# Kernel optimization log

Measured on AMD Instinct MI355X. Metric: run time of the kernel, lower is better.

The kernel has to match this reference:

```python
import jax, jax.numpy as jnp
import numpy as np

B, T, M_DIM, P_DIM = 32, 192, 256, 16
D, HE, HD, HG = 1024, 1024, 1024, 512
NH, DH, DFF, NL = 16, 64, 4096, 8
CTX = 10
E = P_DIM // 2  # num_experts = d_phase // 2
PRELU_A = 0.25  # torch PReLU default init slope (treated as constant)
LN_EPS = 1e-5


def prelu(x):
    return jnp.where(x >= 0, x, PRELU_A * x)


def layer_norm(x, g, b):
    m = x.mean(-1, keepdims=True)
    v = ((x - m) ** 2).mean(-1, keepdims=True)
    return (x - m) * jax.lax.rsqrt(v + LN_EPS) * g + b


def setup_inputs() -> dict:
    key = jax.random.key(0)
    ks = iter(jax.random.split(key, 64))
    w = lambda *s: jax.random.normal(next(ks), s, jnp.float32) * 0.02
    return dict(
        motion=jax.random.normal(next(ks), (B, T, M_DIM), jnp.float32),
        phase=jax.random.normal(next(ks), (B, T, P_DIM), jnp.float32),
        enc_W1=w(M_DIM + 1 + P_DIM, HE), enc_b1=w(HE), enc_W2=w(HE, D), enc_b2=w(D),
        kf_W1=w(2, D), kf_b1=w(D), kf_W2=w(D, D), kf_b2=w(D),
        rp_W1=w(1, DH), rp_b1=w(DH), rp_W2=w(DH, DH), rp_b2=w(DH),
        att_Wq=w(NL, D, NH * DH), att_bq=w(NL, NH * DH),
        att_Wk=w(NL, D, NH * DH), att_bk=w(NL, NH * DH),
        att_Wv=w(NL, D, NH * DH), att_bv=w(NL, NH * DH),
        att_Wo=w(NL, NH * DH, D), att_bo=w(NL, D),
        att_ln_g=jnp.ones((NL, D)), att_ln_b=jnp.zeros((NL, D)),
        pff_W1=w(NL, D, DFF), pff_b1=w(NL, DFF),
        pff_W2=w(NL, DFF, D), pff_b2=w(NL, D),
        pff_ln_g=jnp.ones((NL, D)), pff_ln_b=jnp.zeros((NL, D)),
        fin_ln_g=jnp.ones(D), fin_ln_b=jnp.zeros(D),
        pd_W1=w(D, HD), pd_b1=w(HD), pd_W2=w(HD, P_DIM), pd_b2=w(P_DIM),
        g_W1=w(P_DIM, HG), g_b1=w(HG), g_W2=w(HG, HG), g_b2=w(HG),
        g_W3=w(HG, E), g_b3=w(E),
        md_W0=w(E, D, HD), md_b0=w(E, HD),
        md_W1=w(E, HD, HD), md_b1=w(E, HD),
        md_W2=w(E, HD, M_DIM), md_b2=w(E, M_DIM),
    )


def reference(motion, phase, enc_W1, enc_b1, enc_W2, enc_b2,
              kf_W1, kf_b1, kf_W2, kf_b2, rp_W1, rp_b1, rp_W2, rp_b2,
              att_Wq, att_bq, att_Wk, att_bk, att_Wv, att_bv, att_Wo, att_bo,
              att_ln_g, att_ln_b, pff_W1, pff_b1, pff_W2, pff_b2, pff_ln_g, pff_ln_b,
              fin_ln_g, fin_ln_b, pd_W1, pd_b1, pd_W2, pd_b2,
              g_W1, g_b1, g_W2, g_b2, g_W3, g_b3,
              md_W0, md_b0, md_W1, md_b1, md_W2, md_b2):
    frames = jnp.arange(T)
    # eval mode: no midway targets; keyframes = context frames + last frame
    key_mask = (frames < CTX) | (frames == T - 1)          # [T]
    dm = key_mask.astype(motion.dtype)[:, None]            # data mask [T,1]
    x = jnp.concatenate([motion * dm,
                         jnp.broadcast_to(dm, (B, T, 1)),
                         phase * dm], axis=-1)
    x = prelu(x @ enc_W1 + enc_b1)
    x = prelu(x @ enc_W2 + enc_b2)                          # [B,T,D]
    # keyframe position embedding (distance to last context / target frame)
    ctx_idx = (frames - (CTX - 1)).astype(x.dtype)
    tgt_idx = -(frames - (T - 1)).astype(x.dtype)
    kp = jnp.stack([ctx_idx, tgt_idx], axis=-1)            # [T,2]
    x = x + (prelu(kp @ kf_W1 + kf_b1) @ kf_W2 + kf_b2)
    # relative position embedding, offsets -(T-1)..(T-1)
    rp = jnp.arange(-T + 1, T, dtype=x.dtype)[:, None]     # [2T-1,1]
    rel = prelu(rp @ rp_W1 + rp_b1) @ rp_W2 + rp_b2        # [2T-1,DH]
    rel_idx = frames[None, :] - frames[:, None] + (T - 1)  # [T,T] -> index into 2T-1
    blocked = ~key_mask                                    # attention mask: only attend to keyframes
    neg = jnp.asarray(-1e9, x.dtype)
    scale = 1.0 / np.sqrt(DH)

    def block(x, p):
        Wq, bq, Wk, bk, Wv, bv, Wo, bo, lg, lb, pW1, pb1, pW2, pb2, plg, plb = p
        h = layer_norm(x, lg, lb)                          # pre_lnorm
        q = (h @ Wq + bq).reshape(B, T, NH, DH)
        k = (h @ Wk + bk).reshape(B, T, NH, DH)
        v = (h @ Wv + bv).reshape(B, T, NH, DH)
        ac = jnp.einsum('bind,bjnd->bnij', q, k)           # content score
        bd = jnp.einsum('bind,rd->bnir', q, rel)           # rel-pos score (shared across heads' rel emb)
        bd = jnp.take_along_axis(bd, jnp.broadcast_to(rel_idx[None, None], ac.shape), axis=-1)
        s = (ac + bd) * scale
        s = jnp.where(blocked[None, None, None, :], neg, s)
        a = jax.nn.softmax(s, axis=-1)
        o = jnp.einsum('bnij,bjnd->bind', a, v).reshape(B, T, NH * DH)
        x = x + o @ Wo + bo
        h2 = layer_norm(x, plg, plb)
        x = x + jax.nn.relu(h2 @ pW1 + pb1) @ pW2 + pb2    # positionwise FF
        return x, None

    layer_params = (att_Wq, att_bq, att_Wk, att_bk, att_Wv, att_bv, att_Wo, att_bo,
                    att_ln_g, att_ln_b, pff_W1, pff_b1, pff_W2, pff_b2, pff_ln_g, pff_ln_b)
    x, _ = jax.lax.scan(block, x, layer_params)
    x = layer_norm(x, fin_ln_g, fin_ln_b)                  # final LN (pre_lnorm)
    # phase decoder
    phase_out = prelu(x @ pd_W1 + pd_b1) @ pd_W2 + pd_b2   # [B,T,P]
    # gating network -> per-frame soft expert weights
    h = prelu(phase_out @ g_W1 + g_b1)
    h = prelu(h @ g_W2 + g_b2)
    gate = jax.nn.softmax(h @ g_W3 + g_b3, axis=-1)        # [B,T,E]

    def mlin(y, W, b):
        # MultiLinear + per-frame expert blend: sum_e gate_e * (y @ W_e + b_e)
        return jnp.einsum('btd,edh,bte->bth', y, W, gate) + jnp.einsum('bte,eh->bth', gate, b)

    y = prelu(mlin(x, md_W0, md_b0))
    y = prelu(mlin(y, md_W1, md_b1))
    y = mlin(y, md_W2, md_b2)                              # [B,T,M]
    return y, phase_out
```

## Files before the change

### kernel.cpp

```cpp
#include <hip/hip_runtime.h>
#include <stdint.h>

typedef unsigned short u16;
typedef __attribute__((ext_vector_type(4))) float f32x4;
typedef __attribute__((ext_vector_type(8))) __bf16 bf16x8;

#define NT 6144
#define TT 192
#define PRELU_A 0.25f

__device__ __forceinline__ u16 f2bf(float f) {
  unsigned u = __float_as_uint(f);
  u += 0x7fffu + ((u >> 16) & 1u);
  return (u16)(u >> 16);
}
__device__ __forceinline__ float bf2f(u16 u) {
  return __uint_as_float(((unsigned)u) << 16);
}

__device__ __forceinline__ void gload16(const u16* g, __bf16* l) {
  auto* l3 = reinterpret_cast<__attribute__((address_space(3))) __bf16*>(
      reinterpret_cast<uintptr_t>(l));
  const auto* g1 = reinterpret_cast<const __attribute__((address_space(1))) u16*>(
      reinterpret_cast<uintptr_t>(g));
  __builtin_amdgcn_global_load_lds(g1, l3, 16, 0, 0);
}

__device__ __forceinline__ void xcd_remap(int& bx, int& by)
{
  const int gx = gridDim.x, gy = gridDim.y;
  const int nwg = gx * gy;
  const int f = blockIdx.y * gx + blockIdx.x;
  const int q = nwg >> 3, r = nwg & 7;
  const int xcd = f & 7, s = f >> 3;
  const int w = (xcd < r ? xcd*(q+1) : r*(q+1) + (xcd-r)*q) + s;
  const int CX = ((gx & 7) == 0) ? (gx >> 3) : 1;
  const int per = gy * CX;
  const int c = w / per, rr = w - c*per;
  bx = c*CX + (rr % CX);
  by = rr / CX;
}

struct TrDesc {
  const float* src; u16* dst;
  int K, N, Kp, Np;
  int tilesX, perBatch, batch, tileOff;
  long sstride, dstride;
};
struct TrTable { TrDesc d[18]; int n; };

__global__ __launch_bounds__(256)
void transpose_all(TrTable T)
{
  __shared__ float tile[64][65];
  const int bid = blockIdx.x;
  TrDesc de;
  #pragma unroll 1
  for (int i = 0; i < T.n; ++i) {
    const TrDesc& e = T.d[i];
    if (bid >= e.tileOff && bid < e.tileOff + e.perBatch * e.batch) { de = e; break; }
  }
  const int local = bid - de.tileOff;
  const int z = local / de.perBatch;
  const int rem = local - z * de.perBatch;
  const int ty = rem / de.tilesX;
  const int tx = rem - ty * de.tilesX;
  const float* src = de.src + (long)z * de.sstride;
  u16* dst = de.dst + (long)z * de.dstride;
  const int kt = ty * 64, nt2 = tx * 64;

  if (kt + 64 <= de.K && nt2 + 64 <= de.N) {
    #pragma unroll
    for (int i = 0; i < 4; ++i) {
      const int flat = threadIdx.x + i*256;
      const int ng = (flat & 7) | (((flat >> 9) & 1) << 3);
      const int kl = ((flat >> 3) & 7) | (((flat >> 6) & 7) << 3);
      const float4 v = *(const float4*)(src + (long)(kt + kl)*de.N + nt2 + ng*4);
      *(float4*)&tile[kl][ng*4] = v;
    }
  } else {
    #pragma unroll
    for (int i = 0; i < 16; ++i) {
      int idx = threadIdx.x + i*256;
      int kl = idx >> 6, nl = idx & 63;
      int k = kt + kl, n = nt2 + nl;
      tile[kl][nl] = (k < de.K && n < de.N) ? src[(long)k*de.N + n] : 0.f;
    }
  }
  __syncthreads();
  #pragma unroll
  for (int i = 0; i < 4; ++i) {
    const int flat = threadIdx.x + i*256;
    const int kg = (flat & 7) | (((flat >> 5) & 1) << 3);
    const int nl = ((flat >> 3) & 3) | (((flat >> 6) & 15) << 2);
    ushort4 o;
    o.x = f2bf(tile[kg*4 + 0][nl]);
    o.y = f2bf(tile[kg*4 + 1][nl]);
    o.z = f2bf(tile[kg*4 + 2][nl]);
    o.w = f2bf(tile[kg*4 + 3][nl]);
    *(ushort4*)(dst + (long)(nt2 + nl)*de.Kp + kt + kg*4) = o;
  }
}

template<int MR, int HM>
__device__ __forceinline__ void epilogue_store(
    f32x4 (&acc)[MR][4], long arow0, long brow0, int wm, int wn, int lane,
    const float* bias, int biasN,
    float* Cf, int ldc, int Nf, int accum,
    u16* Cb, int ldcb, int Nb, int act, const float* radd)
{
  const int rbase = wm*HM + ((lane >> 4) << 2);
  const int cbase = wn*64 + (lane & 15);
  #pragma unroll
  for (int m = 0; m < MR; ++m) {
    #pragma unroll
    for (int n = 0; n < 4; ++n) {
      const long gcol = brow0 + cbase + n*16;
      const float bv = (bias && gcol < biasN) ? bias[gcol] : 0.f;
      #pragma unroll
      for (int r = 0; r < 4; ++r) {
        const long grow = arow0 + rbase + m*16 + r;
        float v = acc[m][n][r] + bv;
        if (act == 1) v = fmaxf(v, 0.f);
        else if (act == 2) v = (v >= 0.f) ? v : PRELU_A * v;
        if (radd) v += radd[(int)(grow % TT)*1024 + gcol];
        if (Cf && gcol < Nf) {
          const long idx = grow * (long)ldc + gcol;
          Cf[idx] = accum ? (Cf[idx] + v) : v;
        }
        if (Cb && gcol < Nb) Cb[grow * (long)ldcb + gcol] = f2bf(v);
      }
    }
  }
}

__global__ __launch_bounds__(256, 3)
void gemm64(const u16* __restrict__ A, const u16* __restrict__ Bt,
            const float* __restrict__ bias, int biasN,
            float* __restrict__ Cf, int ldc, int Nf, int accum,
            u16* __restrict__ Cb, int ldcb, int Nb,
            int K, int act, const float* __restrict__ radd)
{
  __shared__ __bf16 As[2*64*64];
  __shared__ __bf16 Bs[2*128*64];
  const int tid = threadIdx.x;
  const int wid = tid >> 6;
  const int lane = tid & 63;
  const int wm = wid >> 1, wn = wid & 1;
  int bx, by; xcd_remap(bx, by);
  const long arow0 = (long)bx * 64;
  const long brow0 = (long)by * 128;
  const int lr  = lane >> 3;
  const int lko = ((lane & 7) ^ (lane >> 3)) << 3;

  f32x4 acc[2][4];
  #pragma unroll
  for (int m = 0; m < 2; ++m)
    #pragma unroll
    for (int n = 0; n < 4; ++n) acc[m][n] = (f32x4)0.f;

  const int aro = lane & 15;
  const int g = lane >> 4;

  auto stage = [&](int buf, int kt) {
    #pragma unroll
    for (int c = wid; c < 24; c += 4) {
      if (c < 8) gload16(A + (arow0 + c*8 + lr)*K + kt + lko, As + buf*(64*64) + c*512);
      else       gload16(Bt + (brow0 + (c-8)*8 + lr)*K + kt + lko,
                         Bs + buf*(128*64) + (c-8)*512);
    }
  };

  const int nt = K >> 6;
  stage(0, 0);
  for (int t = 0; t < nt; ++t) {
    if (t + 1 < nt) {
      stage((t+1) & 1, (t+1) << 6);
      asm volatile("s_waitcnt vmcnt(6)" ::: "memory");
    } else {
      asm volatile("s_waitcnt vmcnt(0)" ::: "memory");
    }
    __builtin_amdgcn_s_barrier();
    asm volatile("" ::: "memory");
    const __bf16* Ab = As + (t&1)*(64*64);
    const __bf16* Bb = Bs + (t&1)*(128*64);
    #pragma unroll
    for (int kk = 0; kk < 2; ++kk) {
      bf16x8 af[2], bfv[4];
      #pragma unroll
      for (int m = 0; m < 2; ++m) {
        const int R = wm*32 + m*16 + aro;
        af[m] = *(const bf16x8*)(Ab + R*64 + (((kk*4 + g) ^ (R & 7)) << 3));
      }
      #pragma unroll
      for (int n = 0; n < 4; ++n) {
        const int R = wn*64 + n*16 + aro;
        bfv[n] = *(const bf16x8*)(Bb + R*64 + (((kk*4 + g) ^ (R & 7)) << 3));
      }
      #pragma unroll
      for (int m = 0; m < 2; ++m)
        #pragma unroll
        for (int n = 0; n < 4; ++n)
          acc[m][n] = __builtin_amdgcn_mfma_f32_16x16x32_bf16(af[m], bfv[n], acc[m][n], 0, 0, 0);
    }
    asm volatile("" ::: "memory");
    __builtin_amdgcn_s_barrier();
  }
  epilogue_store<2,32>(acc, arow0, brow0, wm, wn, lane,
                       bias, biasN, Cf, ldc, Nf, accum, Cb, ldcb, Nb, act, radd);
}

__global__ __launch_bounds__(256, 4)
void gemm128(const u16* __restrict__ A, const u16* __restrict__ Bt,
             const float* __restrict__ bias, int biasN,
             float* __restrict__ Cf, int ldc, int Nf, int accum,
             u16* __restrict__ Cb, int ldcb, int Nb,
             int K, int act)
{
  __shared__ __bf16 As[2*128*32];
  __shared__ __bf16 Bs[2*128*32];
  const int tid = threadIdx.x;
  const int wid = tid >> 6;
  const int lane = tid & 63;
  const int wm = wid >> 1, wn = wid & 1;
  int bx, by; xcd_remap(bx, by);
  const long arow0 = (long)bx * 128;
  const long brow0 = (long)by * 128;
  const int srow = lane >> 2;
  const int skoff = ((lane & 3) ^ ((lane >> 3) & 3)) << 3;

  f32x4 acc[4][4];
  #pragma unroll
  for (int m = 0; m < 4; ++m)
    #pragma unroll
    for (int n = 0; n < 4; ++n) acc[m][n] = (f32x4)0.f;

  const int aro = lane & 15;
  const int g = lane >> 4;

  auto stage = [&](int buf, int kt) {
    #pragma unroll
    for (int c = wid; c < 16; c += 4) {
      if (c < 8) gload16(A + (arow0 + c*16 + srow)*K + kt + skoff, As + buf*4096 + c*512);
      else       gload16(Bt + (brow0 + (c-8)*16 + srow)*K + kt + skoff,
                         Bs + buf*4096 + (c-8)*512);
    }
  };

  const int nt = K >> 5;
  stage(0, 0);
  for (int t = 0; t < nt; ++t) {
    if (t + 1 < nt) {
      stage((t+1) & 1, (t+1) << 5);
      asm volatile("s_waitcnt vmcnt(4)" ::: "memory");
    } else {
      asm volatile("s_waitcnt vmcnt(0)" ::: "memory");
    }
    __builtin_amdgcn_s_barrier();
    asm volatile("" ::: "memory");
    const __bf16* Ab = As + (t&1)*4096;
    const __bf16* Bb = Bs + (t&1)*4096;
    bf16x8 af[4], bfv[4];
    #pragma unroll
    for (int m = 0; m < 4; ++m) {
      const int R = wm*64 + m*16 + aro;
      af[m] = *(const bf16x8*)(Ab + R*32 + ((g ^ ((R >> 1) & 3)) << 3));
    }
    #pragma unroll
    for (int n = 0; n < 4; ++n) {
      const int R = wn*64 + n*16 + aro;
      bfv[n] = *(const bf16x8*)(Bb + R*32 + ((g ^ ((R >> 1) & 3)) << 3));
    }
    #pragma unroll
    for (int m = 0; m < 4; ++m)
      #pragma unroll
      for (int n = 0; n < 4; ++n)
        acc[m][n] = __builtin_amdgcn_mfma_f32_16x16x32_bf16(af[m], bfv[n], acc[m][n], 0, 0, 0);
    asm volatile("" ::: "memory");
    __builtin_amdgcn_s_barrier();
  }
  epilogue_store<4,64>(acc, arow0, brow0, wm, wn, lane,
                       bias, biasN, Cf, ldc, Nf, accum, Cb, ldcb, Nb, act, nullptr);
}

__global__ __launch_bounds__(256)
void moe_blend2(const u16* __restrict__ C0, const u16* __restrict__ C1,
                const float* __restrict__ gate, u16* __restrict__ outb)
{
  const long idx = (long)blockIdx.x*256 + threadIdx.x;
  if (idx >= (long)NT*256) return;
  const long t = idx >> 8;
  const int h = (int)(idx & 255) << 2;
  float sx = 0.f, sy = 0.f, sz = 0.f, sw = 0.f;
  #pragma unroll
  for (int j = 0; j < 4; ++j) {
    const float gv = gate[t*8 + j];
    const ushort4 c4 = *(const ushort4*)(C0 + t*4096 + j*1024 + h);
    sx += gv * bf2f(c4.x); sy += gv * bf2f(c4.y);
    sz += gv * bf2f(c4.z); sw += gv * bf2f(c4.w);
  }
  #pragma unroll
  for (int j = 0; j < 4; ++j) {
    const float gv = gate[t*8 + 4 + j];
    const ushort4 c4 = *(const ushort4*)(C1 + t*4096 + j*1024 + h);
    sx += gv * bf2f(c4.x); sy += gv * bf2f(c4.y);
    sz += gv * bf2f(c4.z); sw += gv * bf2f(c4.w);
  }
  sx = (sx >= 0.f) ? sx : PRELU_A * sx;
  sy = (sy >= 0.f) ? sy : PRELU_A * sy;
  sz = (sz >= 0.f) ? sz : PRELU_A * sz;
  sw = (sw >= 0.f) ? sw : PRELU_A * sw;
  ushort4 o; o.x = f2bf(sx); o.y = f2bf(sy); o.z = f2bf(sz); o.w = f2bf(sw);
  *(ushort4*)(outb + t*1024 + h) = o;
}

__global__ __launch_bounds__(256)
void moe_blend_out(const u16* __restrict__ C, const float* __restrict__ gate,
                   float* __restrict__ outf)
{
  const long idx = (long)blockIdx.x*256 + threadIdx.x;
  if (idx >= (long)NT*64) return;
  const long t = idx >> 6;
  const int h = (int)(idx & 63) << 2;
  float sx = 0.f, sy = 0.f, sz = 0.f, sw = 0.f;
  #pragma unroll
  for (int j = 0; j < 8; ++j) {
    const float gv = gate[t*8 + j];
    const ushort4 c4 = *(const ushort4*)(C + t*2048 + j*256 + h);
    sx += gv * bf2f(c4.x); sy += gv * bf2f(c4.y);
    sz += gv * bf2f(c4.z); sw += gv * bf2f(c4.w);
  }
  float4 o; o.x = sx; o.y = sy; o.z = sz; o.w = sw;
  ((float4*)(outf + t*256))[h >> 2] = o;
}

__global__ __launch_bounds__(256)
void build_xin(const float* __restrict__ motion, const float* __restrict__ phase,
               u16* __restrict__ xin)
{
  const long idx = (long)blockIdx.x*256 + threadIdx.x;
  if (idx >= (long)NT*320) return;
  const int c = (int)(idx % 320);
  const long row = idx / 320;
  const int t = (int)(row % TT);
  const bool dm = (t < 10) || (t == TT-1);
  float v;
  if (c < 256)       v = dm ? motion[row*256 + c] : 0.f;
  else if (c == 256) v = dm ? 1.f : 0.f;
  else if (c < 273)  v = dm ? phase[row*16 + (c-257)] : 0.f;
  else               v = 0.f;
  xin[idx] = f2bf(v);
}

__global__ __launch_bounds__(256)
void build_kp_kvb(u16* __restrict__ kp,
                  const float* __restrict__ bk, const float* __restrict__ bv,
                  float* __restrict__ kvb)
{
  const int idx = blockIdx.x*256 + threadIdx.x;
  if (idx < 256*64) {
    const int r = idx / 64, c = idx % 64;
    float v = 0.f;
    if (r < TT) {
      if (c == 0) v = (float)(r - 9);
      else if (c == 1) v = (float)(TT-1 - r);
    }
    kp[idx] = f2bf(v);
  } else {
    const int j = idx - 256*64;
    if (j < 8*2048) {
      const int l = j >> 11, c = j & 2047;
      kvb[j] = (c < 1024) ? bk[l*1024 + c] : bv[l*1024 + c - 1024];
    }
  }
}

__global__ __launch_bounds__(64)
void relpos(const float* __restrict__ W1, const float* __restrict__ b1,
            const float* __restrict__ W2, const float* __restrict__ b2,
            float* __restrict__ rel)
{
  const int r = blockIdx.x;
  const int d = threadIdx.x;
  __shared__ float h[64];
  const float rp = (float)(r - (TT-1));
  float hv = rp * W1[d] + b1[d];
  hv = (hv >= 0.f) ? hv : PRELU_A * hv;
  h[d] = hv;
  __syncthreads();
  if (r < 2*TT - 1) {
    float o = b2[d];
    for (int j = 0; j < 64; ++j) o += h[j] * W2[j*64 + d];
    rel[r*64 + d] = o;
  } else {
    rel[r*64 + d] = 0.f;
  }
}

__global__ __launch_bounds__(256)
void ln_bf16(const float* __restrict__ x, const float* __restrict__ g,
             const float* __restrict__ b, u16* __restrict__ out,
             u16* __restrict__ hk)
{
  const long row = blockIdx.x;
  const float4 v = ((const float4*)(x + row*1024))[threadIdx.x];
  float s  = v.x + v.y + v.z + v.w;
  float s2 = v.x*v.x + v.y*v.y + v.z*v.z + v.w*v.w;
  #pragma unroll
  for (int m = 32; m; m >>= 1) { s += __shfl_xor(s, m); s2 += __shfl_xor(s2, m); }
  __shared__ float red[8];
  const int wid = threadIdx.x >> 6;
  if ((threadIdx.x & 63) == 0) { red[wid] = s; red[wid+4] = s2; }
  __syncthreads();
  s  = red[0] + red[1] + red[2] + red[3];
  s2 = red[4] + red[5] + red[6] + red[7];
  const float mean = s * (1.f/1024.f);
  const float var  = fmaxf(s2 * (1.f/1024.f) - mean*mean, 0.f);
  const float rs   = rsqrtf(var + 1e-5f);
  const float4 gg = ((const float4*)g)[threadIdx.x];
  const float4 bb = ((const float4*)b)[threadIdx.x];
  ushort4 o;
  o.x = f2bf((v.x-mean)*rs*gg.x + bb.x);
  o.y = f2bf((v.y-mean)*rs*gg.y + bb.y);
  o.z = f2bf((v.z-mean)*rs*gg.z + bb.z);
  o.w = f2bf((v.w-mean)*rs*gg.w + bb.w);
  ((ushort4*)(out + row*1024))[threadIdx.x] = o;
  if (hk) {
    const int t = (int)(row % TT);
    if (t < 10 || t == TT-1) {
      const int bidx = (int)(row / TT);
      const int j = (t < 10) ? t : 10;
      ((ushort4*)(hk + (long)(bidx*11 + j)*1024))[threadIdx.x] = o;
    }
  }
}

__global__ __launch_bounds__(256)
void attn11(const float* __restrict__ q, const float* __restrict__ kv,
            const float* __restrict__ rel, u16* __restrict__ o)
{
  const int row = blockIdx.x;
  const int b = row / TT, i = row - b*TT;
  const int t = threadIdx.x;
  const int n = t >> 4;
  const int dq = t & 15;
  const float4 qv = *(const float4*)(q + (long)row*1024 + t*4);
  float e[11];
  float mx = -1e30f;
  #pragma unroll
  for (int j = 0; j < 11; ++j) {
    const int kf = (j < 10) ? j : (TT-1);
    const float4 k4 = *(const float4*)(kv + (long)(b*11 + j)*2048 + n*64 + dq*4);
    const float4 r4 = *(const float4*)(rel + (kf - i + TT-1)*64 + dq*4);
    float s = qv.x*(k4.x+r4.x) + qv.y*(k4.y+r4.y)
            + qv.z*(k4.z+r4.z) + qv.w*(k4.w+r4.w);
    s += __shfl_xor(s, 1); s += __shfl_xor(s, 2);
    s += __shfl_xor(s, 4); s += __shfl_xor(s, 8);
    e[j] = s * 0.125f;
    mx = fmaxf(mx, e[j]);
  }
  float den = 0.f;
  #pragma unroll
  for (int j = 0; j < 11; ++j) { e[j] = __expf(e[j] - mx); den += e[j]; }
  const float inv = 1.f / den;
  float ax = 0.f, ay = 0.f, az = 0.f, aw = 0.f;
  #pragma unroll
  for (int j = 0; j < 11; ++j) {
    const float4 v4 = *(const float4*)(kv + (long)(b*11 + j)*2048 + 1024 + n*64 + dq*4);
    ax += e[j]*v4.x; ay += e[j]*v4.y; az += e[j]*v4.z; aw += e[j]*v4.w;
  }
  ushort4 ov;
  ov.x = f2bf(ax*inv); ov.y = f2bf(ay*inv); ov.z = f2bf(az*inv); ov.w = f2bf(aw*inv);
  *(ushort4*)(o + (long)row*1024 + t*4) = ov;
}

__global__ __launch_bounds__(256)
void softmax8(const float* __restrict__ lg, float* __restrict__ gate)
{
  const int t = blockIdx.x*256 + threadIdx.x;
  if (t >= NT) return;
  float v[8], mx = -1e30f;
  #pragma unroll
  for (int e = 0; e < 8; ++e) { v[e] = lg[t*8 + e]; mx = fmaxf(mx, v[e]); }
  float den = 0.f;
  #pragma unroll
  for (int e = 0; e < 8; ++e) { v[e] = __expf(v[e] - mx); den += v[e]; }
  const float inv = 1.f / den;
  #pragma unroll
  for (int e = 0; e < 8; ++e) gate[t*8 + e] = v[e] * inv;
}

extern "C" void kernel_launch(void* const* d_in, const int* in_sizes, int n_in,
                              void* d_out, int out_size, void* d_ws, size_t ws_size,
                              hipStream_t stream)
{
  (void)in_sizes; (void)n_in; (void)out_size; (void)ws_size;
  const float* motion  = (const float*)d_in[0];
  const float* phase   = (const float*)d_in[1];
  const float* enc_W1  = (const float*)d_in[2];
  const float* enc_b1  = (const float*)d_in[3];
  const float* enc_W2  = (const float*)d_in[4];
  const float* enc_b2  = (const float*)d_in[5];
  const float* kf_W1   = (const float*)d_in[6];
  const float* kf_b1   = (const float*)d_in[7];
  const float* kf_W2   = (const float*)d_in[8];
  const float* kf_b2   = (const float*)d_in[9];
  const float* rp_W1   = (const float*)d_in[10];
  const float* rp_b1   = (const float*)d_in[11];
  const float* rp_W2   = (const float*)d_in[12];
  const float* rp_b2   = (const float*)d_in[13];
  const float* att_Wq  = (const float*)d_in[14];
  const float* att_bq  = (const float*)d_in[15];
  const float* att_Wk  = (const float*)d_in[16];
  const float* att_bk  = (const float*)d_in[17];
  const float* att_Wv  = (const float*)d_in[18];
  const float* att_bv  = (const float*)d_in[19];
  const float* att_Wo  = (const float*)d_in[20];
  const float* att_bo  = (const float*)d_in[21];
  const float* att_ln_g = (const float*)d_in[22];
  const float* att_ln_b = (const float*)d_in[23];
  const float* pff_W1  = (const float*)d_in[24];
  const float* pff_b1  = (const float*)d_in[25];
  const float* pff_W2  = (const float*)d_in[26];
  const float* pff_b2  = (const float*)d_in[27];
  const float* pff_ln_g = (const float*)d_in[28];
  const float* pff_ln_b = (const float*)d_in[29];
  const float* fin_ln_g = (const float*)d_in[30];
  const float* fin_ln_b = (const float*)d_in[31];
  const float* pd_W1   = (const float*)d_in[32];
  const float* pd_b1   = (const float*)d_in[33];
  const float* pd_W2   = (const float*)d_in[34];
  const float* pd_b2   = (const float*)d_in[35];
  const float* g_W1    = (const float*)d_in[36];
  const float* g_b1    = (const float*)d_in[37];
  const float* g_W2    = (const float*)d_in[38];
  const float* g_b2    = (const float*)d_in[39];
  const float* g_W3    = (const float*)d_in[40];
  const float* g_b3    = (const float*)d_in[41];
  const float* md_W0   = (const float*)d_in[42];
  const float* md_b0   = (const float*)d_in[43];
  const float* md_W1   = (const float*)d_in[44];
  const float* md_b1   = (const float*)d_in[45];
  const float* md_W2   = (const float*)d_in[46];
  const float* md_b2   = (const float*)d_in[47];

  char* wsp = (char*)d_ws;
  size_t off = 0;
  auto alloc = [&](size_t bytes) -> char* {
    char* p = wsp + off;
    off += (bytes + 255) & ~(size_t)255;
    return p;
  };

  u16* encW1T = (u16*)alloc((size_t)1024*320*2);
  u16* encW2T = (u16*)alloc((size_t)1024*1024*2);
  u16* kfW1T  = (u16*)alloc((size_t)1024*64*2);
  u16* kfW2T  = (u16*)alloc((size_t)1024*1024*2);
  u16* WqT    = (u16*)alloc((size_t)8*1024*1024*2);
  u16* kvT    = (u16*)alloc((size_t)8*2048*1024*2);
  u16* WoT    = (u16*)alloc((size_t)8*1024*1024*2);
  u16* F1T    = (u16*)alloc((size_t)8*4096*1024*2);
  u16* F2T    = (u16*)alloc((size_t)8*1024*4096*2);
  u16* pdW1T  = (u16*)alloc((size_t)1024*1024*2);
  u16* pdW2T  = (u16*)alloc((size_t)128*1024*2);
  u16* gW1T   = (u16*)alloc((size_t)512*64*2);
  u16* gW2T   = (u16*)alloc((size_t)512*512*2);
  u16* gW3T   = (u16*)alloc((size_t)128*512*2);
  u16* md0T   = (u16*)alloc((size_t)8*1024*1024*2);
  u16* md1T   = (u16*)alloc((size_t)8*1024*1024*2);
  u16* md2T   = (u16*)alloc((size_t)8*256*1024*2);

  float* x    = (float*)alloc((size_t)NT*1024*4);
  float* rel  = (float*)alloc((size_t)384*64*4);
  u16*   kp   = (u16*)  alloc((size_t)256*64*2);
  u16*   kf1  = (u16*)  alloc((size_t)256*1024*2);
  float* kfe  = (float*)alloc((size_t)256*1024*4);
  u16*   hk   = (u16*)  alloc((size_t)384*1024*2);
  float* kvb  = (float*)alloc((size_t)8*2048*4);
  float* kvbuf= (float*)alloc((size_t)384*2048*4);
  u16*   phbf = (u16*)  alloc((size_t)NT*64*2);
  float* glog = (float*)alloc((size_t)NT*8*4);
  float* gate = (float*)alloc((size_t)NT*8*4);
  u16*   xin  = (u16*)  alloc((size_t)NT*320*2);
  u16*   s1   = (u16*)  alloc((size_t)NT*1024*2);
  float* s2   = (float*)alloc((size_t)NT*1024*4);
  u16*   s3   = (u16*)  alloc((size_t)NT*1024*2);
  u16*   s4   = (u16*)  alloc((size_t)NT*4096*2);
  u16*   s5   = (u16*)  alloc((size_t)NT*4096*2);

  float* outY = (float*)d_out;
  float* outP = outY + (size_t)NT*256;

  auto g64 = [&](const u16* A, const u16* Bt, const float* bias, int biasN,
                 float* Cf, int ldc, int Nf, int accum,
                 u16* Cb, int ldcb, int Nb, int M, int K, int Npad, int act,
                 const float* radd) {
    gemm64<<<dim3(M/64, Npad/128), 256, 0, stream>>>(
        A, Bt, bias, biasN, Cf, ldc, Nf, accum, Cb, ldcb, Nb, K, act, radd);
  };
  auto g128 = [&](const u16* A, const u16* Bt, const float* bias, int biasN,
                  float* Cf, int ldc, int Nf, int accum,
                  u16* Cb, int ldcb, int Nb, int M, int K, int Npad, int act) {
    gemm128<<<dim3(M/128, Npad/128), 256, 0, stream>>>(
        A, Bt, bias, biasN, Cf, ldc, Nf, accum, Cb, ldcb, Nb, K, act);
  };

  TrTable T;
  int tn = 0, toff = 0;
  auto addtr = [&](const float* s_, u16* d_, int K, int N, int Kp, int Np,
                   int batch, long dstride) {
    TrDesc& e = T.d[tn++];
    e.src = s_; e.dst = d_; e.K = K; e.N = N; e.Kp = Kp; e.Np = Np;
    e.tilesX = (Np + 63) / 64;
    e.perBatch = e.tilesX * ((Kp + 63) / 64);
    e.batch = batch; e.tileOff = toff;
    e.sstride = (long)K * N; e.dstride = dstride;
    toff += e.perBatch * batch;
  };
  addtr(enc_W1, encW1T, 273, 1024, 320, 1024, 1, (long)1024*320);
  addtr(enc_W2, encW2T, 1024, 1024, 1024, 1024, 1, (long)1024*1024);
  addtr(kf_W1,  kfW1T,  2, 1024, 64, 1024, 1, (long)1024*64);
  addtr(kf_W2,  kfW2T,  1024, 1024, 1024, 1024, 1, (long)1024*1024);
  addtr(att_Wq, WqT, 1024, 1024, 1024, 1024, 8, (long)1024*1024);
  addtr(att_Wk, kvT,                      1024, 1024, 1024, 1024, 8, (long)2048*1024);
  addtr(att_Wv, kvT + (size_t)1024*1024,  1024, 1024, 1024, 1024, 8, (long)2048*1024);
  addtr(att_Wo, WoT, 1024, 1024, 1024, 1024, 8, (long)1024*1024);
  addtr(pff_W1, F1T, 1024, 4096, 1024, 4096, 8, (long)4096*1024);
  addtr(pff_W2, F2T, 4096, 1024, 4096, 1024, 8, (long)1024*4096);
  addtr(pd_W1,  pdW1T, 1024, 1024, 1024, 1024, 1, (long)1024*1024);
  addtr(pd_W2,  pdW2T, 1024, 16, 1024, 128, 1, (long)128*1024);
  addtr(g_W1,   gW1T, 16, 512, 64, 512, 1, (long)512*64);
  addtr(g_W2,   gW2T, 512, 512, 512, 512, 1, (long)512*512);
  addtr(g_W3,   gW3T, 512, 8, 512, 128, 1, (long)128*512);
  addtr(md_W0,  md0T, 1024, 1024, 1024, 1024, 8, (long)1024*1024);
  addtr(md_W1,  md1T, 1024, 1024, 1024, 1024, 8, (long)1024*1024);
  addtr(md_W2,  md2T, 1024, 256, 1024, 256, 8, (long)256*1024);
  T.n = tn;
  transpose_all<<<toff, 256, 0, stream>>>(T);

  build_xin<<<(NT*320 + 255)/256, 256, 0, stream>>>(motion, phase, xin);
  build_kp_kvb<<<(256*64 + 8*2048 + 255)/256, 256, 0, stream>>>(kp, att_bk, att_bv, kvb);
  relpos<<<384, 64, 0, stream>>>(rp_W1, rp_b1, rp_W2, rp_b2, rel);

  g64(kp,  kfW1T, kf_b1, 1024, nullptr,0,0,0, kf1,1024,1024, 256, 64, 1024, 2, nullptr);
  g64(kf1, kfW2T, kf_b2, 1024, kfe,1024,1024,0, nullptr,0,0, 256, 1024, 1024, 0, nullptr);
  g64(xin, encW1T, enc_b1, 1024, nullptr,0,0,0, s1,1024,1024, NT, 320, 1024, 2, nullptr);
  g64(s1,  encW2T, enc_b2, 1024, x,1024,1024,0, nullptr,0,0, NT, 1024, 1024, 2, kfe);

  for (int l = 0; l < 8; ++l) {
    const size_t w1 = (size_t)l*1024*1024;
    const size_t wf = (size_t)l*4096*1024;
    ln_bf16<<<NT, 256, 0, stream>>>(x, att_ln_g + l*1024, att_ln_b + l*1024, s1, hk);
    g64(s1, WqT + w1, att_bq + l*1024, 1024, s2,1024,1024,0, nullptr,0,0, NT, 1024, 1024, 0, nullptr);
    g64(hk, kvT + (size_t)l*2048*1024, kvb + l*2048, 2048,
        kvbuf,2048,2048,0, nullptr,0,0, 384, 1024, 2048, 0, nullptr);
    attn11<<<NT, 256, 0, stream>>>(s2, kvbuf, rel, s3);
    g64(s3, WoT + w1, att_bo + l*1024, 1024, x,1024,1024,1, nullptr,0,0, NT, 1024, 1024, 0, nullptr);
    ln_bf16<<<NT, 256, 0, stream>>>(x, pff_ln_g + l*1024, pff_ln_b + l*1024, s1, nullptr);
    g128(s1, F1T + wf, pff_b1 + l*4096, 4096, nullptr,0,0,0, s4,4096,4096, NT, 1024, 4096, 1);
    g64(s4, F2T + wf, pff_b2 + l*1024, 1024, x,1024,1024,1, nullptr,0,0, NT, 4096, 1024, 0, nullptr);
  }

  ln_bf16<<<NT, 256, 0, stream>>>(x, fin_ln_g, fin_ln_b, s1, nullptr);
  g64(s1, pdW1T, pd_b1, 1024, nullptr,0,0,0, s3,1024,1024, NT, 1024, 1024, 2, nullptr);
  g64(s3, pdW2T, pd_b2, 16, outP,16,16,0, phbf,64,64, NT, 1024, 128, 0, nullptr);

  g64(phbf, gW1T, g_b1, 512, nullptr,0,0,0, s3,512,512, NT, 64, 512, 2, nullptr);
  g64(s3,   gW2T, g_b2, 512, nullptr,0,0,0, s4,512,512, NT, 512, 512, 2, nullptr);
  g64(s4,   gW3T, g_b3, 8,  glog,8,8,0, nullptr,0,0, NT, 512, 128, 0, nullptr);
  softmax8<<<(NT + 255)/256, 256, 0, stream>>>(glog, gate);

  const int BL2 = (int)(((long)NT*256 + 255)/256);
  g128(s1, md0T,                     md_b0,        4096, nullptr,0,0,0, s4,4096,4096, NT, 1024, 4096, 0);
  g128(s1, md0T + (size_t)4096*1024, md_b0 + 4096, 4096, nullptr,0,0,0, s5,4096,4096, NT, 1024, 4096, 0);
  moe_blend2<<<BL2, 256, 0, stream>>>(s4, s5, gate, s3);
  g128(s3, md1T,                     md_b1,        4096, nullptr,0,0,0, s4,4096,4096, NT, 1024, 4096, 0);
  g128(s3, md1T + (size_t)4096*1024, md_b1 + 4096, 4096, nullptr,0,0,0, s5,4096,4096, NT, 1024, 4096, 0);
  moe_blend2<<<BL2, 256, 0, stream>>>(s4, s5, gate, s1);
  g128(s1, md2T, md_b2, 2048, nullptr,0,0,0, s4,2048,2048, NT, 1024, 2048, 0);
  moe_blend_out<<<(int)(((long)NT*64 + 255)/256), 256, 0, stream>>>(s4, gate, outY);
}
```

Before: 2.941 ms.

## Fuse Q and KV projections into one launch, store Q as bf16, batch expert GEMMs

The Q projection and the keyframe KV projection now run as a single gemm64qkv launch that splits its flat block index between the two problems. Q is written as bf16 instead of fp32, which halves its write and read traffic, and attn11 converts it back on load. The paired MoE expert GEMMs use a grid z dimension to cover both halves in one launch. Together these remove launch gaps and tail underutilisation and reduce memory traffic, at the cost of slightly lower precision for Q.

New measurement: 2.792 ms (median of 2 runs). 5.1% less time.

```diff
diff --git a/kernel.cpp b/kernel.cpp
--- a/kernel.cpp
+++ b/kernel.cpp
@@ -26,19 +26,25 @@
   __builtin_amdgcn_global_load_lds(g1, l3, 16, 0, 0);
 }
 
-__device__ __forceinline__ void xcd_remap(int& bx, int& by)
-{
-  const int gx = gridDim.x, gy = gridDim.y;
-  const int nwg = gx * gy;
-  const int f = blockIdx.y * gx + blockIdx.x;
+__device__ __forceinline__ int remap_flat(int f, int nwg)
+{
   const int q = nwg >> 3, r = nwg & 7;
   const int xcd = f & 7, s = f >> 3;
-  const int w = (xcd < r ? xcd*(q+1) : r*(q+1) + (xcd-r)*q) + s;
+  return (xcd < r ? xcd*(q+1) : r*(q+1) + (xcd-r)*q) + s;
+}
+__device__ __forceinline__ void decode_st(int w, int gx, int gy, int& bx, int& by)
+{
   const int CX = ((gx & 7) == 0) ? (gx >> 3) : 1;
   const int per = gy * CX;
   const int c = w / per, rr = w - c*per;
   bx = c*CX + (rr % CX);
   by = rr / CX;
+}
+__device__ __forceinline__ void xcd_remap(int& bx, int& by)
+{
+  const int gx = gridDim.x, gy = gridDim.y;
+  const int w = remap_flat(blockIdx.y * gx + blockIdx.x, gx * gy);
+  decode_st(w, gx, gy, bx, by);
 }
 
 struct TrDesc {
@@ -134,20 +140,18 @@
   }
 }
 
-__global__ __launch_bounds__(256, 3)
-void gemm64(const u16* __restrict__ A, const u16* __restrict__ Bt,
-            const float* __restrict__ bias, int biasN,
-            float* __restrict__ Cf, int ldc, int Nf, int accum,
-            u16* __restrict__ Cb, int ldcb, int Nb,
-            int K, int act, const float* __restrict__ radd)
-{
-  __shared__ __bf16 As[2*64*64];
-  __shared__ __bf16 Bs[2*128*64];
+__device__ __forceinline__ void gemm64_body(
+    const u16* __restrict__ A, const u16* __restrict__ Bt,
+    const float* __restrict__ bias, int biasN,
+    float* __restrict__ Cf, int ldc, int Nf, int accum,
+    u16* __restrict__ Cb, int ldcb, int Nb,
+    int K, int act, const float* __restrict__ radd,
+    int bx, int by, __bf16* As, __bf16* Bs)
+{
   const int tid = threadIdx.x;
   const int wid = tid >> 6;
   const int lane = tid & 63;
   const int wm = wid >> 1, wn = wid & 1;
-  int bx, by; xcd_remap(bx, by);
   const long arow0 = (long)bx * 64;
   const long brow0 = (long)by * 128;
   const int lr  = lane >> 3;
@@ -210,15 +214,51 @@
                        bias, biasN, Cf, ldc, Nf, accum, Cb, ldcb, Nb, act, radd);
 }
 
+__global__ __launch_bounds__(256, 3)
+void gemm64(const u16* __restrict__ A, const u16* __restrict__ Bt,
+            const float* __restrict__ bias, int biasN,
+            float* __restrict__ Cf, int ldc, int Nf, int accum,
+            u16* __restrict__ Cb, int ldcb, int Nb,
+            int K, int act, const float* __restrict__ radd)
+{
+  __shared__ __bf16 As[2*64*64];
+  __shared__ __bf16 Bs[2*128*64];
+  int bx, by; xcd_remap(bx, by);
+  gemm64_body(A, Bt, bias, biasN, Cf, ldc, Nf, accum, Cb, ldcb, Nb,
+              K, act, radd, bx, by, As, Bs);
+}
+
+__global__ __launch_bounds__(256, 3)
+void gemm64qkv(const u16* __restrict__ Aq, const u16* __restrict__ WqTl,
+               const float* __restrict__ bq,  u16* __restrict__ qbf,
+               const u16* __restrict__ Akv, const u16* __restrict__ kvTl,
+               const float* __restrict__ kvbl, float* __restrict__ kvbuf)
+{
+  __shared__ __bf16 As[2*64*64];
+  __shared__ __bf16 Bs[2*128*64];
+  const int w = remap_flat(blockIdx.x, 864);
+  int bx, by;
+  if (w < 768) {
+    decode_st(w, 96, 8, bx, by);
+    gemm64_body(Aq, WqTl, bq, 1024, nullptr, 0, 0, 0, qbf, 1024, 1024,
+                1024, 0, nullptr, bx, by, As, Bs);
+  } else {
+    decode_st(w - 768, 6, 16, bx, by);
+    gemm64_body(Akv, kvTl, kvbl, 2048, kvbuf, 2048, 2048, 0, nullptr, 0, 0,
+                1024, 0, nullptr, bx, by, As, Bs);
+  }
+}
+
 __global__ __launch_bounds__(256, 4)
 void gemm128(const u16* __restrict__ A, const u16* __restrict__ Bt,
              const float* __restrict__ bias, int biasN,
              float* __restrict__ Cf, int ldc, int Nf, int accum,
              u16* __restrict__ Cb, int ldcb, int Nb,
-             int K, int act)
+             int K, int act, long btoff, u16* __restrict__ Cb2)
 {
   __shared__ __bf16 As[2*128*32];
   __shared__ __bf16 Bs[2*128*32];
+  if (blockIdx.z) { Bt += btoff; bias += biasN; Cb = Cb2; }
   const int tid = threadIdx.x;
   const int wid = tid >> 6;
   const int lane = tid & 63;
@@ -436,7 +476,7 @@
 }
 
 __global__ __launch_bounds__(256)
-void attn11(const float* __restrict__ q, const float* __restrict__ kv,
+void attn11(const u16* __restrict__ q, const float* __restrict__ kv,
             const float* __restrict__ rel, u16* __restrict__ o)
 {
   const int row = blockIdx.x;
@@ -444,7 +484,9 @@
   const int t = threadIdx.x;
   const int n = t >> 4;
   const int dq = t & 15;
-  const float4 qv = *(const float4*)(q + (long)row*1024 + t*4);
+  const ushort4 qu = *(const ushort4*)(q + (long)row*1024 + t*4);
+  float4 qv;
+  qv.x = bf2f(qu.x); qv.y = bf2f(qu.y); qv.z = bf2f(qu.z); qv.w = bf2f(qu.w);
   float e[11];
   float mx = -1e30f;
   #pragma unroll
@@ -583,7 +625,7 @@
   float* gate = (float*)alloc((size_t)NT*8*4);
   u16*   xin  = (u16*)  alloc((size_t)NT*320*2);
   u16*   s1   = (u16*)  alloc((size_t)NT*1024*2);
-  float* s2   = (float*)alloc((size_t)NT*1024*4);
+  u16*   qbf  = (u16*)  alloc((size_t)NT*1024*2);
   u16*   s3   = (u16*)  alloc((size_t)NT*1024*2);
   u16*   s4   = (u16*)  alloc((size_t)NT*4096*2);
   u16*   s5   = (u16*)  alloc((size_t)NT*4096*2);
@@ -600,9 +642,10 @@
   };
   auto g128 = [&](const u16* A, const u16* Bt, const float* bias, int biasN,
                   float* Cf, int ldc, int Nf, int accum,
-                  u16* Cb, int ldcb, int Nb, int M, int K, int Npad, int act) {
-    gemm128<<<dim3(M/128, Npad/128), 256, 0, stream>>>(
-        A, Bt, bias, biasN, Cf, ldc, Nf, accum, Cb, ldcb, Nb, K, act);
+                  u16* Cb, int ldcb, int Nb, int M, int K, int Npad, int act,
+                  int zn, long btoff, u16* Cb2) {
+    gemm128<<<dim3(M/128, Npad/128, zn), 256, 0, stream>>>(
+        A, Bt, bias, biasN, Cf, ldc, Nf, accum, Cb, ldcb, Nb, K, act, btoff, Cb2);
   };
 
   TrTable T;
@@ -651,13 +694,13 @@
     const size_t w1 = (size_t)l*1024*1024;
     const size_t wf = (size_t)l*4096*1024;
     ln_bf16<<<NT, 256, 0, stream>>>(x, att_ln_g + l*1024, att_ln_b + l*1024, s1, hk);
-    g64(s1, WqT + w1, att_bq + l*1024, 1024, s2,1024,1024,0, nullptr,0,0, NT, 1024, 1024, 0, nullptr);
-    g64(hk, kvT + (size_t)l*2048*1024, kvb + l*2048, 2048,
-        kvbuf,2048,2048,0, nullptr,0,0, 384, 1024, 2048, 0, nullptr);
-    attn11<<<NT, 256, 0, stream>>>(s2, kvbuf, rel, s3);
+    gemm64qkv<<<864, 256, 0, stream>>>(
+        s1, WqT + w1, att_bq + l*1024, qbf,
+        hk, kvT + (size_t)l*2048*1024, kvb + l*2048, kvbuf);
+    attn11<<<NT, 256, 0, stream>>>(qbf, kvbuf, rel, s3);
     g64(s3, WoT + w1, att_bo + l*1024, 1024, x,1024,1024,1, nullptr,0,0, NT, 1024, 1024, 0, nullptr);
     ln_bf16<<<NT, 256, 0, stream>>>(x, pff_ln_g + l*1024, pff_ln_b + l*1024, s1, nullptr);
-    g128(s1, F1T + wf, pff_b1 + l*4096, 4096, nullptr,0,0,0, s4,4096,4096, NT, 1024, 4096, 1);
+    g128(s1, F1T + wf, pff_b1 + l*4096, 4096, nullptr,0,0,0, s4,4096,4096, NT, 1024, 4096, 1, 1, 0, nullptr);
     g64(s4, F2T + wf, pff_b2 + l*1024, 1024, x,1024,1024,1, nullptr,0,0, NT, 4096, 1024, 0, nullptr);
   }
 
@@ -671,12 +714,13 @@
   softmax8<<<(NT + 255)/256, 256, 0, stream>>>(glog, gate);
 
   const int BL2 = (int)(((long)NT*256 + 255)/256);
-  g128(s1, md0T,                     md_b0,        4096, nullptr,0,0,0, s4,4096,4096, NT, 1024, 4096, 0);
-  g128(s1, md0T + (size_t)4096*1024, md_b0 + 4096, 4096, nullptr,0,0,0, s5,4096,4096, NT, 1024, 4096, 0);
+  g128(s1, md0T, md_b0, 4096, nullptr,0,0,0, s4,4096,4096, NT, 1024, 4096, 0,
+       2, (long)4096*1024, s5);
   moe_blend2<<<BL2, 256, 0, stream>>>(s4, s5, gate, s3);
-  g128(s3, md1T,                     md_b1,        4096, nullptr,0,0,0, s4,4096,4096, NT, 1024, 4096, 0);
-  g128(s3, md1T + (size_t)4096*1024, md_b1 + 4096, 4096, nullptr,0,0,0, s5,4096,4096, NT, 1024, 4096, 0);
+  g128(s3, md1T, md_b1, 4096, nullptr,0,0,0, s4,4096,4096, NT, 1024, 4096, 0,
+       2, (long)4096*1024, s5);
   moe_blend2<<<BL2, 256, 0, stream>>>(s4, s5, gate, s1);
-  g128(s1, md2T, md_b2, 2048, nullptr,0,0,0, s4,2048,2048, NT, 1024, 2048, 0);
+  g128(s1, md2T, md_b2, 2048, nullptr,0,0,0, s4,2048,2048, NT, 1024, 2048, 0,
+       1, 0, nullptr);
   moe_blend_out<<<(int)(((long)NT*64 + 255)/256), 256, 0, stream>>>(s4, gate, outY);
 }
```
